# Kernel optimization log

Hardware: AMD Instinct MI355X
Metric: run time of the kernel (lower is better)

## Reference

```python
import jax, jax.numpy as jnp
import numpy as np

EMBED_DIM = 1024
NUM_HEADS = 16
HEAD_DIM = EMBED_DIM // NUM_HEADS
SCALING = HEAD_DIM ** -0.5
TGT_LEN, BSZ = 2048, 2


def setup_inputs() -> dict:
    key = jax.random.key(0)
    k1, k2, k3 = jax.random.split(key, 3)
    return {
        "query": jax.random.normal(k1, (TGT_LEN, BSZ, EMBED_DIM), jnp.float32),
        "in_proj_weight": jax.random.normal(k2, (3 * EMBED_DIM, EMBED_DIM), jnp.float32) * (EMBED_DIM ** -0.5),
        "in_proj_bias": jnp.zeros((3 * EMBED_DIM,), jnp.float32),
        "out_w": jax.random.normal(k3, (EMBED_DIM, EMBED_DIM), jnp.float32) * (EMBED_DIM ** -0.5),
        "out_b": jnp.zeros((EMBED_DIM,), jnp.float32),
    }


def reference(query, in_proj_weight, in_proj_bias, out_w, out_b):
    tgt_len, bsz, embed_dim = query.shape
    # fused QKV projection (self-attention path: qkv_same)
    qkv = query @ in_proj_weight.T + in_proj_bias  # [T, B, 3E]
    q, k, v = jnp.split(qkv, 3, axis=-1)
    q = q * SCALING
    # [T, B, E] -> [B*H, T, hd]
    def to_heads(x):
        return x.reshape(tgt_len, bsz * NUM_HEADS, HEAD_DIM).transpose(1, 0, 2)
    q, k, v = to_heads(q), to_heads(k), to_heads(v)
    attn_weights = jnp.einsum('bqd,bkd->bqk', q, k)          # [B*H, T, T]
    attn_weights = jax.nn.softmax(attn_weights, axis=-1)
    attn = jnp.einsum('bqk,bkd->bqd', attn_weights, v)       # [B*H, T, hd]
    attn = attn.transpose(1, 0, 2).reshape(tgt_len, bsz, embed_dim)
    attn = attn @ out_w.T + out_b
    # averaged attention weights over heads (need_weights=True)
    avg_weights = attn_weights.reshape(bsz, NUM_HEADS, tgt_len, tgt_len).mean(axis=1)
    return attn, avg_weights
```

## Files before the change

### kernel.cpp

```cpp
#include <hip/hip_runtime.h>
#include <hip/hip_bf16.h>
#include <math.h>

#define T_LEN 2048
#define BSZ   2
#define EMB   1024
#define NH    16
#define HD    64
#define BHN   (BSZ*NH)
#define M1    (T_LEN*BSZ)
#define SCAL  0.125f
#define QSCALE (0.125f * 1.44269504088896f)

typedef __attribute__((ext_vector_type(8))) short bf16x8;
typedef __attribute__((ext_vector_type(4))) float f32x4;

__device__ inline unsigned short f2bf(float x) {
    union { float f; unsigned u; } v; v.f = x;
    unsigned r = v.u + 0x7FFF + ((v.u >> 16) & 1);
    return (unsigned short)(r >> 16);
}

__device__ inline unsigned pack2bf(float a, float b) {
    union { __hip_bfloat162 h; unsigned u; } v;
    v.h = __float22bfloat162_rn(make_float2(a, b));
    return v.u;
}

__device__ inline float fexp2(float x) {
#if __has_builtin(__builtin_amdgcn_exp2f)
    return __builtin_amdgcn_exp2f(x);
#else
    return exp2f(x);
#endif
}

__device__ inline void async16(const unsigned short* g, unsigned short* l) {
    __builtin_amdgcn_global_load_lds(
        (const __attribute__((address_space(1))) void*)g,
        (__attribute__((address_space(3))) void*)l, 16, 0, 0);
}

__device__ inline unsigned short* swz(unsigned short* base, int r, int c) {
    return base + (((r << 3) + (c ^ (r & 7))) << 3);
}
__device__ inline const unsigned short* swz(const unsigned short* base, int r, int c) {
    return base + (((r << 3) + (c ^ (r & 7))) << 3);
}

__global__ __launch_bounds__(256) void cvt_bf16_kernel(
    const float* __restrict__ src, unsigned short* __restrict__ dst, int n8)
{
    int idx = blockIdx.x * 256 + threadIdx.x;
    if (idx >= n8) return;
    float4 a = reinterpret_cast<const float4*>(src)[idx * 2];
    float4 b = reinterpret_cast<const float4*>(src)[idx * 2 + 1];
    unsigned o[4] = { pack2bf(a.x, a.y), pack2bf(a.z, a.w),
                      pack2bf(b.x, b.y), pack2bf(b.z, b.w) };
    reinterpret_cast<uint4*>(dst)[idx] = *reinterpret_cast<uint4*>(o);
}

__global__ __launch_bounds__(256) void qkv_mfma_kernel(
    const unsigned short* __restrict__ A, const unsigned short* __restrict__ B,
    const float* __restrict__ bias,
    unsigned short* __restrict__ Q16, unsigned short* __restrict__ K16,
    unsigned short* __restrict__ Vt16)
{
    constexpr int BM = 128, BN = 128, BK = 32, K = 1024;
    __shared__ unsigned short As[BM * BK];
    __shared__ unsigned short Bs[BN * BK];
    const int tid = threadIdx.x;
    const int lane = tid & 63, wave = tid >> 6;
    const int quad = lane >> 4, l16 = lane & 15;
    const int wr = wave >> 1, wc = wave & 1;
    const int m0 = blockIdx.x * BM, n0 = blockIdx.y * BN;

    f32x4 zero4 = {0.f, 0.f, 0.f, 0.f};
    f32x4 acc[4][4];
    #pragma unroll
    for (int i = 0; i < 4; ++i)
        #pragma unroll
        for (int j = 0; j < 4; ++j) acc[i][j] = zero4;

    for (int k0 = 0; k0 < K; k0 += BK) {
        __syncthreads();
        #pragma unroll
        for (int t = 0; t < 2; ++t) {
            int c = t * 256 + tid;
            int m = c >> 2, kb = c & 3;
            async16(&A[(size_t)(m0 + m) * K + k0 + kb * 8], &As[c * 8]);
            async16(&B[(size_t)(n0 + m) * K + k0 + kb * 8], &Bs[c * 8]);
        }
        __syncthreads();
        bf16x8 af[4], bfr[4];
        #pragma unroll
        for (int i = 0; i < 4; ++i) {
            af[i]  = *reinterpret_cast<const bf16x8*>(&As[(wr * 64 + i * 16 + l16) * BK + quad * 8]);
            bfr[i] = *reinterpret_cast<const bf16x8*>(&Bs[(wc * 64 + i * 16 + l16) * BK + quad * 8]);
        }
        #pragma unroll
        for (int i = 0; i < 4; ++i)
            #pragma unroll
            for (int j = 0; j < 4; ++j)
                acc[i][j] = __builtin_amdgcn_mfma_f32_16x16x32_bf16(af[i], bfr[j], acc[i][j], 0, 0, 0);
    }

    #pragma unroll
    for (int j = 0; j < 4; ++j) {
        int n = n0 + wc * 64 + j * 16 + l16;
        float bv = bias[n];
        int which = n >> 10;
        int c = n & 1023;
        int h = c >> 6, d = c & 63;
        #pragma unroll
        for (int i = 0; i < 4; ++i) {
            #pragma unroll
            for (int r = 0; r < 4; ++r) {
                int m = m0 + wr * 64 + i * 16 + quad * 4 + r;
                int t = m >> 1, b = m & 1;
                int bh = b * NH + h;
                float v = acc[i][j][r] + bv;
                if (which == 0)      Q16[((size_t)bh * T_LEN + t) * HD + d] = f2bf(v * QSCALE);
                else if (which == 1) K16[((size_t)bh * T_LEN + t) * HD + d] = f2bf(v);
                else                 Vt16[((size_t)bh * HD + d) * T_LEN + t] = f2bf(v);
            }
        }
    }
}

__global__ __launch_bounds__(256) void flash_mfma_kernel(
    const unsigned short* __restrict__ Qb, const unsigned short* __restrict__ Kb,
    const unsigned short* __restrict__ Vt, unsigned short* __restrict__ AO,
    float* __restrict__ Lrow)
{
    __shared__ unsigned short Ks[64 * 64];
    __shared__ unsigned short Vs[64 * 64];
    __shared__ unsigned short Ps[128 * 64];
    const int tid = threadIdx.x;
    const int lane = tid & 63, wave = tid >> 6;
    const int quad = lane >> 4, l16 = lane & 15;
    const int qt = blockIdx.x, bh = blockIdx.y;
    const int q0 = qt * 128;
    const int b = bh >> 4, h = bh & 15;

    bf16x8 qf[2][2];
    #pragma unroll
    for (int s = 0; s < 2; ++s) {
        const unsigned short* Qp =
            Qb + ((size_t)bh * T_LEN + q0 + wave * 32 + s * 16 + l16) * HD;
        qf[s][0] = *reinterpret_cast<const bf16x8*>(Qp + quad * 8);
        qf[s][1] = *reinterpret_cast<const bf16x8*>(Qp + 32 + quad * 8);
    }

    f32x4 zero4 = {0.f, 0.f, 0.f, 0.f};
    f32x4 oacc[4][2];
    #pragma unroll
    for (int dt = 0; dt < 4; ++dt) { oacc[dt][0] = zero4; oacc[dt][1] = zero4; }
    float l_i[2] = {0.f, 0.f};

    const unsigned short* Kbase = Kb + (size_t)bh * T_LEN * HD;
    const unsigned short* Vbase = Vt + (size_t)bh * HD * T_LEN;

    const int cl0 = tid, cl1 = tid + 256;
    const int r0 = cl0 >> 3, c0 = (cl0 & 7) ^ (r0 & 7);
    const int r1 = cl1 >> 3, c1 = (cl1 & 7) ^ (r1 & 7);

    for (int kt = 0; kt < T_LEN; kt += 64) {
        __syncthreads();
        async16(&Kbase[(size_t)(kt + r0) * HD + c0 * 8], &Ks[cl0 * 8]);
        async16(&Kbase[(size_t)(kt + r1) * HD + c1 * 8], &Ks[cl1 * 8]);
        async16(&Vbase[(size_t)r0 * T_LEN + kt + c0 * 8], &Vs[cl0 * 8]);
        async16(&Vbase[(size_t)r1 * T_LEN + kt + c1 * 8], &Vs[cl1 * 8]);
        __syncthreads();

        f32x4 sacc[2][4];
        #pragma unroll
        for (int kb = 0; kb < 4; ++kb) { sacc[0][kb] = zero4; sacc[1][kb] = zero4; }
        #pragma unroll
        for (int kb = 0; kb < 4; ++kb) {
            bf16x8 kf0 = *reinterpret_cast<const bf16x8*>(swz(Ks, kb * 16 + l16, quad));
            sacc[0][kb] = __builtin_amdgcn_mfma_f32_16x16x32_bf16(kf0, qf[0][0], sacc[0][kb], 0, 0, 0);
            sacc[1][kb] = __builtin_amdgcn_mfma_f32_16x16x32_bf16(kf0, qf[1][0], sacc[1][kb], 0, 0, 0);
            bf16x8 kf1 = *reinterpret_cast<const bf16x8*>(swz(Ks, kb * 16 + l16, 4 + quad));
            sacc[0][kb] = __builtin_amdgcn_mfma_f32_16x16x32_bf16(kf1, qf[0][1], sacc[0][kb], 0, 0, 0);
            sacc[1][kb] = __builtin_amdgcn_mfma_f32_16x16x32_bf16(kf1, qf[1][1], sacc[1][kb], 0, 0, 0);
        }

        #pragma unroll
        for (int s = 0; s < 2; ++s) {
            const int Rp = wave * 32 + s * 16 + l16;
            float psum = 0.f;
            #pragma unroll
            for (int kb = 0; kb < 4; ++kb) {
                float p0 = fexp2(sacc[s][kb][0]);
                float p1 = fexp2(sacc[s][kb][1]);
                float p2 = fexp2(sacc[s][kb][2]);
                float p3 = fexp2(sacc[s][kb][3]);
                psum += (p0 + p1) + (p2 + p3);
                unsigned o[2] = { pack2bf(p0, p1), pack2bf(p2, p3) };
                *reinterpret_cast<uint2*>(
                    swz(Ps, Rp, 2 * kb + (quad >> 1)) + (quad & 1) * 4) =
                    *reinterpret_cast<uint2*>(o);
            }
            psum += __shfl_xor(psum, 16);
            psum += __shfl_xor(psum, 32);
            l_i[s] += psum;
        }

        #pragma unroll
        for (int st = 0; st < 2; ++st) {
            bf16x8 pb0 = *reinterpret_cast<const bf16x8*>(swz(Ps, wave * 32 + l16, st * 4 + quad));
            bf16x8 pb1 = *reinterpret_cast<const bf16x8*>(swz(Ps, wave * 32 + 16 + l16, st * 4 + quad));
            #pragma unroll
            for (int dt = 0; dt < 4; ++dt) {
                bf16x8 va = *reinterpret_cast<const bf16x8*>(swz(Vs, dt * 16 + l16, st * 4 + quad));
                oacc[dt][0] = __builtin_amdgcn_mfma_f32_16x16x32_bf16(va, pb0, oacc[dt][0], 0, 0, 0);
                oacc[dt][1] = __builtin_amdgcn_mfma_f32_16x16x32_bf16(va, pb1, oacc[dt][1], 0, 0, 0);
            }
        }
    }

    #pragma unroll
    for (int s = 0; s < 2; ++s) {
        float rl = 1.0f / l_i[s];
        int q = q0 + wave * 32 + s * 16 + l16;
        size_t base = ((size_t)q * BSZ + b) * EMB + h * HD;
        #pragma unroll
        for (int dt = 0; dt < 4; ++dt) {
            unsigned o[2] = { pack2bf(oacc[dt][0][s ? 0 : 0] * 0.f + oacc[dt][s][0] * rl,
                                      oacc[dt][s][1] * rl),
                              pack2bf(oacc[dt][s][2] * rl, oacc[dt][s][3] * rl) };
            *reinterpret_cast<uint2*>(&AO[base + dt * 16 + quad * 4]) = *reinterpret_cast<uint2*>(o);
        }
        if (quad == 0)
            Lrow[(size_t)bh * T_LEN + q] = rl;
    }
}

__global__ __launch_bounds__(256) void avg_mfma_kernel(
    const unsigned short* __restrict__ Qb, const unsigned short* __restrict__ Kb,
    const float* __restrict__ Lrow, float* __restrict__ avg_out)
{
    __shared__ unsigned short Ks[64 * 64];
    const int tid = threadIdx.x;
    const int lane = tid & 63, wave = tid >> 6;
    const int quad = lane >> 4, l16 = lane & 15;
    const int kt = blockIdx.x, qt = blockIdx.y, b = blockIdx.z;
    const int q0 = qt * 64, k0 = kt * 64;

    const int cl0 = tid, cl1 = tid + 256;
    const int r0 = cl0 >> 3, c0 = (cl0 & 7) ^ (r0 & 7);
    const int r1 = cl1 >> 3, c1 = (cl1 & 7) ^ (r1 & 7);

    f32x4 zero4 = {0.f, 0.f, 0.f, 0.f};
    f32x4 acc[4] = {zero4, zero4, zero4, zero4};

    for (int h = 0; h < NH; ++h) {
        int bh = b * NH + h;
        __syncthreads();
        const unsigned short* Kg = Kb + ((size_t)bh * T_LEN + k0) * HD;
        async16(&Kg[(size_t)r0 * HD + c0 * 8], &Ks[cl0 * 8]);
        async16(&Kg[(size_t)r1 * HD + c1 * 8], &Ks[cl1 * 8]);
        __syncthreads();

        const unsigned short* Qp = Qb + ((size_t)bh * T_LEN + q0 + wave * 16 + l16) * HD;
        bf16x8 qf0 = *reinterpret_cast<const bf16x8*>(Qp + quad * 8);
        bf16x8 qf1 = *reinterpret_cast<const bf16x8*>(Qp + 32 + quad * 8);

        f32x4 sacc[4] = {zero4, zero4, zero4, zero4};
        #pragma unroll
        for (int c = 0; c < 4; ++c) {
            bf16x8 kb0 = *reinterpret_cast<const bf16x8*>(swz(Ks, c * 16 + l16, quad));
            sacc[c] = __builtin_amdgcn_mfma_f32_16x16x32_bf16(qf0, kb0, sacc[c], 0, 0, 0);
            bf16x8 kb1 = *reinterpret_cast<const bf16x8*>(swz(Ks, c * 16 + l16, 4 + quad));
            sacc[c] = __builtin_amdgcn_mfma_f32_16x16x32_bf16(qf1, kb1, sacc[c], 0, 0, 0);
        }
        #pragma unroll
        for (int r = 0; r < 4; ++r) {
            int q = q0 + wave * 16 + quad * 4 + r;
            float rl = Lrow[(size_t)bh * T_LEN + q];
            #pragma unroll
            for (int c = 0; c < 4; ++c)
                acc[c][r] += fexp2(sacc[c][r]) * rl;
        }
    }
    #pragma unroll
    for (int r = 0; r < 4; ++r) {
        int q = q0 + wave * 16 + quad * 4 + r;
        size_t base = ((size_t)b * T_LEN + q) * T_LEN + k0;
        #pragma unroll
        for (int c = 0; c < 4; ++c)
            avg_out[base + c * 16 + l16] = acc[c][r] * (1.0f / 16.0f);
    }
}

__global__ __launch_bounds__(256) void out_mfma_kernel(
    const unsigned short* __restrict__ A, const unsigned short* __restrict__ B,
    const float* __restrict__ bias, float* __restrict__ out)
{
    constexpr int BM = 128, BN = 128, BK = 32, K = 1024;
    __shared__ unsigned short As[BM * BK];
    __shared__ unsigned short Bs[BN * BK];
    const int tid = threadIdx.x;
    const int lane = tid & 63, wave = tid >> 6;
    const int quad = lane >> 4, l16 = lane & 15;
    const int wr = wave >> 1, wc = wave & 1;
    const int m0 = blockIdx.x * BM, n0 = blockIdx.y * BN;

    f32x4 zero4 = {0.f, 0.f, 0.f, 0.f};
    f32x4 acc[4][4];
    #pragma unroll
    for (int i = 0; i < 4; ++i)
        #pragma unroll
        for (int j = 0; j < 4; ++j) acc[i][j] = zero4;

    for (int k0 = 0; k0 < K; k0 += BK) {
        __syncthreads();
        #pragma unroll
        for (int t = 0; t < 2; ++t) {
            int c = t * 256 + tid;
            int m = c >> 2, kb = c & 3;
            async16(&A[(size_t)(m0 + m) * K + k0 + kb * 8], &As[c * 8]);
            async16(&B[(size_t)(n0 + m) * K + k0 + kb * 8], &Bs[c * 8]);
        }
        __syncthreads();
        bf16x8 af[4], bfr[4];
        #pragma unroll
        for (int i = 0; i < 4; ++i) {
            af[i]  = *reinterpret_cast<const bf16x8*>(&As[(wr * 64 + i * 16 + l16) * BK + quad * 8]);
            bfr[i] = *reinterpret_cast<const bf16x8*>(&Bs[(wc * 64 + i * 16 + l16) * BK + quad * 8]);
        }
        #pragma unroll
        for (int i = 0; i < 4; ++i)
            #pragma unroll
            for (int j = 0; j < 4; ++j)
                acc[i][j] = __builtin_amdgcn_mfma_f32_16x16x32_bf16(af[i], bfr[j], acc[i][j], 0, 0, 0);
    }

    #pragma unroll
    for (int j = 0; j < 4; ++j) {
        int n = n0 + wc * 64 + j * 16 + l16;
        float bv = bias[n];
        #pragma unroll
        for (int i = 0; i < 4; ++i) {
            #pragma unroll
            for (int r = 0; r < 4; ++r) {
                int m = m0 + wr * 64 + i * 16 + quad * 4 + r;
                out[(size_t)m * 1024 + n] = acc[i][j][r] + bv;
            }
        }
    }
}

extern "C" void kernel_launch(void* const* d_in, const int* in_sizes, int n_in,
                              void* d_out, int out_size, void* d_ws, size_t ws_size,
                              hipStream_t stream)
{
    const float* query = (const float*)d_in[0];
    const float* wqkv  = (const float*)d_in[1];
    const float* bqkv  = (const float*)d_in[2];
    const float* wout  = (const float*)d_in[3];
    const float* bout  = (const float*)d_in[4];
    float* out = (float*)d_out;

    char* ws = (char*)d_ws;
    const size_t E_Q   = (size_t)M1 * EMB;
    const size_t E_W   = (size_t)3 * EMB * EMB;
    const size_t E_WO  = (size_t)EMB * EMB;
    const size_t E_QKV = (size_t)BHN * T_LEN * HD;

    unsigned short* queryb = (unsigned short*)ws;
    unsigned short* wqkvb  = queryb + E_Q;
    unsigned short* woutb  = wqkvb + E_W;
    unsigned short* Q16    = woutb + E_WO;
    unsigned short* K16    = Q16 + E_QKV;
    unsigned short* Vt16   = K16 + E_QKV;
    unsigned short* AO16   = Vt16 + E_QKV;
    float* Lr = (float*)(AO16 + E_Q);
    const size_t need = (E_Q + E_W + E_WO + 4 * E_QKV) * 2 + (size_t)BHN * T_LEN * 4;
    if (ws_size < need) return;

    cvt_bf16_kernel<<<(int)(E_Q / 8 / 256), 256, 0, stream>>>(query, queryb, (int)(E_Q / 8));
    cvt_bf16_kernel<<<(int)(E_W / 8 / 256), 256, 0, stream>>>(wqkv, wqkvb, (int)(E_W / 8));
    cvt_bf16_kernel<<<(int)(E_WO / 8 / 256), 256, 0, stream>>>(wout, woutb, (int)(E_WO / 8));

    qkv_mfma_kernel<<<dim3(M1 / 128, 3072 / 128), 256, 0, stream>>>(queryb, wqkvb, bqkv, Q16, K16, Vt16);
    flash_mfma_kernel<<<dim3(T_LEN / 128, BHN), 256, 0, stream>>>(Q16, K16, Vt16, AO16, Lr);
    avg_mfma_kernel<<<dim3(T_LEN / 64, T_LEN / 64, BSZ), 256, 0, stream>>>(Q16, K16, Lr, out + (size_t)M1 * EMB);
    out_mfma_kernel<<<dim3(M1 / 128, 1024 / 128), 256, 0, stream>>>(AO16, woutb, bout, out);
}
```

Measured before the change: 270.8 us.

## Split flash attention over key halves with combine kernel; double-buffer avg K loads

The flash kernel now splits the key range into two halves across a third grid dimension, so twice as many blocks run. Each block writes unnormalized partial outputs and row sums, and a new combine kernel adds the halves, normalizes, and writes AO and the reciprocal row sums. This relies on the scores having no running max, since the exp2 values from both halves can be added directly. It costs an extra launch, extra partial-buffer traffic, and a bf16 rounding of the partial outputs before normalization. Separately, the averaged-weights kernel double-buffers its per-head K tile loads so the next head's load overlaps compute and one barrier per head is removed.

```diff
diff --git a/kernel.cpp b/kernel.cpp
--- a/kernel.cpp
+++ b/kernel.cpp
@@ -11,6 +11,7 @@
 #define M1    (T_LEN*BSZ)
 #define SCAL  0.125f
 #define QSCALE (0.125f * 1.44269504088896f)
+#define KSPLIT 2
 
 typedef __attribute__((ext_vector_type(8))) short bf16x8;
 typedef __attribute__((ext_vector_type(4))) float f32x4;
@@ -19,6 +20,11 @@
     union { float f; unsigned u; } v; v.f = x;
     unsigned r = v.u + 0x7FFF + ((v.u >> 16) & 1);
     return (unsigned short)(r >> 16);
+}
+
+__device__ inline float bf2f(unsigned short x) {
+    union { unsigned u; float f; } v; v.u = ((unsigned)x) << 16;
+    return v.f;
 }
 
 __device__ inline unsigned pack2bf(float a, float b) {
@@ -130,8 +136,8 @@
 
 __global__ __launch_bounds__(256) void flash_mfma_kernel(
     const unsigned short* __restrict__ Qb, const unsigned short* __restrict__ Kb,
-    const unsigned short* __restrict__ Vt, unsigned short* __restrict__ AO,
-    float* __restrict__ Lrow)
+    const unsigned short* __restrict__ Vt, unsigned short* __restrict__ Opart,
+    float* __restrict__ Lpart)
 {
     __shared__ unsigned short Ks[64 * 64];
     __shared__ unsigned short Vs[64 * 64];
@@ -139,9 +145,10 @@
     const int tid = threadIdx.x;
     const int lane = tid & 63, wave = tid >> 6;
     const int quad = lane >> 4, l16 = lane & 15;
-    const int qt = blockIdx.x, bh = blockIdx.y;
+    const int qt = blockIdx.x, bh = blockIdx.y, ks = blockIdx.z;
     const int q0 = qt * 128;
     const int b = bh >> 4, h = bh & 15;
+    const int kt0 = ks * (T_LEN / KSPLIT), kt1 = kt0 + T_LEN / KSPLIT;
 
     bf16x8 qf[2][2];
     #pragma unroll
@@ -165,7 +172,7 @@
     const int r0 = cl0 >> 3, c0 = (cl0 & 7) ^ (r0 & 7);
     const int r1 = cl1 >> 3, c1 = (cl1 & 7) ^ (r1 & 7);
 
-    for (int kt = 0; kt < T_LEN; kt += 64) {
+    for (int kt = kt0; kt < kt1; kt += 64) {
         __syncthreads();
         async16(&Kbase[(size_t)(kt + r0) * HD + c0 * 8], &Ks[cl0 * 8]);
         async16(&Kbase[(size_t)(kt + r1) * HD + c1 * 8], &Ks[cl1 * 8]);
@@ -222,26 +229,55 @@
 
     #pragma unroll
     for (int s = 0; s < 2; ++s) {
-        float rl = 1.0f / l_i[s];
         int q = q0 + wave * 32 + s * 16 + l16;
-        size_t base = ((size_t)q * BSZ + b) * EMB + h * HD;
+        size_t base = (size_t)ks * M1 * EMB + ((size_t)q * BSZ + b) * EMB + h * HD;
         #pragma unroll
         for (int dt = 0; dt < 4; ++dt) {
-            unsigned o[2] = { pack2bf(oacc[dt][0][s ? 0 : 0] * 0.f + oacc[dt][s][0] * rl,
-                                      oacc[dt][s][1] * rl),
-                              pack2bf(oacc[dt][s][2] * rl, oacc[dt][s][3] * rl) };
-            *reinterpret_cast<uint2*>(&AO[base + dt * 16 + quad * 4]) = *reinterpret_cast<uint2*>(o);
+            unsigned o[2] = { pack2bf(oacc[dt][s][0], oacc[dt][s][1]),
+                              pack2bf(oacc[dt][s][2], oacc[dt][s][3]) };
+            *reinterpret_cast<uint2*>(&Opart[base + dt * 16 + quad * 4]) =
+                *reinterpret_cast<uint2*>(o);
         }
         if (quad == 0)
-            Lrow[(size_t)bh * T_LEN + q] = rl;
-    }
+            Lpart[(size_t)ks * BHN * T_LEN + (size_t)bh * T_LEN + q] = l_i[s];
+    }
+}
+
+__global__ __launch_bounds__(256) void combine_kernel(
+    const unsigned short* __restrict__ Opart, const float* __restrict__ Lpart,
+    unsigned short* __restrict__ AO, float* __restrict__ Lrec)
+{
+    int idx = blockIdx.x * 256 + threadIdx.x;
+    int e8 = idx * 8;
+    int t = e8 >> 11;
+    int rem = e8 & 2047;
+    int b = rem >> 10;
+    int e = rem & 1023;
+    int h = e >> 6;
+    int bh = b * NH + h;
+    size_t lidx = (size_t)bh * T_LEN + t;
+    float l = Lpart[lidx] + Lpart[(size_t)BHN * T_LEN + lidx];
+    float rl = 1.0f / l;
+    uint4 pa = reinterpret_cast<const uint4*>(Opart)[idx];
+    uint4 pb = reinterpret_cast<const uint4*>(Opart)[(size_t)M1 * EMB / 8 + idx];
+    const unsigned short* sa = reinterpret_cast<const unsigned short*>(&pa);
+    const unsigned short* sb = reinterpret_cast<const unsigned short*>(&pb);
+    unsigned o[4];
+    #pragma unroll
+    for (int i = 0; i < 4; ++i) {
+        float v0 = (bf2f(sa[2 * i])     + bf2f(sb[2 * i]))     * rl;
+        float v1 = (bf2f(sa[2 * i + 1]) + bf2f(sb[2 * i + 1])) * rl;
+        o[i] = pack2bf(v0, v1);
+    }
+    reinterpret_cast<uint4*>(AO)[idx] = *reinterpret_cast<uint4*>(o);
+    if ((e & 63) == 0) Lrec[lidx] = rl;
 }
 
 __global__ __launch_bounds__(256) void avg_mfma_kernel(
     const unsigned short* __restrict__ Qb, const unsigned short* __restrict__ Kb,
-    const float* __restrict__ Lrow, float* __restrict__ avg_out)
-{
-    __shared__ unsigned short Ks[64 * 64];
+    const float* __restrict__ Lrec, float* __restrict__ avg_out)
+{
+    __shared__ unsigned short Ks[2][64 * 64];
     const int tid = threadIdx.x;
     const int lane = tid & 63, wave = tid >> 6;
     const int quad = lane >> 4, l16 = lane & 15;
@@ -255,13 +291,21 @@
     f32x4 zero4 = {0.f, 0.f, 0.f, 0.f};
     f32x4 acc[4] = {zero4, zero4, zero4, zero4};
 
+    {
+        const unsigned short* Kg = Kb + ((size_t)(b * NH) * T_LEN + k0) * HD;
+        async16(&Kg[(size_t)r0 * HD + c0 * 8], &Ks[0][cl0 * 8]);
+        async16(&Kg[(size_t)r1 * HD + c1 * 8], &Ks[0][cl1 * 8]);
+    }
+
     for (int h = 0; h < NH; ++h) {
         int bh = b * NH + h;
         __syncthreads();
-        const unsigned short* Kg = Kb + ((size_t)bh * T_LEN + k0) * HD;
-        async16(&Kg[(size_t)r0 * HD + c0 * 8], &Ks[cl0 * 8]);
-        async16(&Kg[(size_t)r1 * HD + c1 * 8], &Ks[cl1 * 8]);
-        __syncthreads();
+        if (h + 1 < NH) {
+            const unsigned short* Kg = Kb + ((size_t)(bh + 1) * T_LEN + k0) * HD;
+            async16(&Kg[(size_t)r0 * HD + c0 * 8], &Ks[(h + 1) & 1][cl0 * 8]);
+            async16(&Kg[(size_t)r1 * HD + c1 * 8], &Ks[(h + 1) & 1][cl1 * 8]);
+        }
+        const unsigned short* Kcur = Ks[h & 1];
 
         const unsigned short* Qp = Qb + ((size_t)bh * T_LEN + q0 + wave * 16 + l16) * HD;
         bf16x8 qf0 = *reinterpret_cast<const bf16x8*>(Qp + quad * 8);
@@ -270,15 +314,15 @@
         f32x4 sacc[4] = {zero4, zero4, zero4, zero4};
         #pragma unroll
         for (int c = 0; c < 4; ++c) {
-            bf16x8 kb0 = *reinterpret_cast<const bf16x8*>(swz(Ks, c * 16 + l16, quad));
+            bf16x8 kb0 = *reinterpret_cast<const bf16x8*>(swz(Kcur, c * 16 + l16, quad));
             sacc[c] = __builtin_amdgcn_mfma_f32_16x16x32_bf16(qf0, kb0, sacc[c], 0, 0, 0);
-            bf16x8 kb1 = *reinterpret_cast<const bf16x8*>(swz(Ks, c * 16 + l16, 4 + quad));
+            bf16x8 kb1 = *reinterpret_cast<const bf16x8*>(swz(Kcur, c * 16 + l16, 4 + quad));
             sacc[c] = __builtin_amdgcn_mfma_f32_16x16x32_bf16(qf1, kb1, sacc[c], 0, 0, 0);
         }
         #pragma unroll
         for (int r = 0; r < 4; ++r) {
             int q = q0 + wave * 16 + quad * 4 + r;
-            float rl = Lrow[(size_t)bh * T_LEN + q];
+            float rl = Lrec[(size_t)bh * T_LEN + q];
             #pragma unroll
             for (int c = 0; c < 4; ++c)
                 acc[c][r] += fexp2(sacc[c][r]) * rl;
@@ -375,9 +419,12 @@
     unsigned short* Q16    = woutb + E_WO;
     unsigned short* K16    = Q16 + E_QKV;
     unsigned short* Vt16   = K16 + E_QKV;
-    unsigned short* AO16   = Vt16 + E_QKV;
-    float* Lr = (float*)(AO16 + E_Q);
-    const size_t need = (E_Q + E_W + E_WO + 4 * E_QKV) * 2 + (size_t)BHN * T_LEN * 4;
+    unsigned short* Opart  = Vt16 + E_QKV;
+    float* Lpart = (float*)(Opart + KSPLIT * E_Q);
+    float* Lrec  = Lpart + (size_t)KSPLIT * BHN * T_LEN;
+    unsigned short* AO16 = queryb;
+    const size_t need = (E_Q + E_W + E_WO + 3 * E_QKV + KSPLIT * E_Q) * 2
+                      + (KSPLIT + 1) * (size_t)BHN * T_LEN * 4;
     if (ws_size < need) return;
 
     cvt_bf16_kernel<<<(int)(E_Q / 8 / 256), 256, 0, stream>>>(query, queryb, (int)(E_Q / 8));
@@ -385,7 +432,8 @@
     cvt_bf16_kernel<<<(int)(E_WO / 8 / 256), 256, 0, stream>>>(wout, woutb, (int)(E_WO / 8));
 
     qkv_mfma_kernel<<<dim3(M1 / 128, 3072 / 128), 256, 0, stream>>>(queryb, wqkvb, bqkv, Q16, K16, Vt16);
-    flash_mfma_kernel<<<dim3(T_LEN / 128, BHN), 256, 0, stream>>>(Q16, K16, Vt16, AO16, Lr);
-    avg_mfma_kernel<<<dim3(T_LEN / 64, T_LEN / 64, BSZ), 256, 0, stream>>>(Q16, K16, Lr, out + (size_t)M1 * EMB);
+    flash_mfma_kernel<<<dim3(T_LEN / 128, BHN, KSPLIT), 256, 0, stream>>>(Q16, K16, Vt16, Opart, Lpart);
+    combine_kernel<<<(int)(E_Q / 8 / 256), 256, 0, stream>>>(Opart, Lpart, AO16, Lrec);
+    avg_mfma_kernel<<<dim3(T_LEN / 64, T_LEN / 64, BSZ), 256, 0, stream>>>(Q16, K16, Lrec, out + (size_t)M1 * EMB);
     out_mfma_kernel<<<dim3(M1 / 128, 1024 / 128), 256, 0, stream>>>(AO16, woutb, bout, out);
 }
```

Result: faster. 261.6 us (-3.4%).
